# Kernel tuning notes

Measured on AMD Instinct MI355X. Metric: run time of the kernel, lower is better.

The kernel has to match this reference:

```python
import jax, jax.numpy as jnp
import numpy as np

NUM_K = 10
T = 1.0  # softmax temperature (forward default)


def setup_inputs() -> dict:
    key = jax.random.key(0)
    k1, k2, k3, k4 = jax.random.split(key, 4)
    B, H, P, D = 64, 12, 197, 64
    return {
        "att_s": jax.random.normal(k1, (B, H, P, P), dtype=jnp.float32),
        "att_t": jax.random.normal(k2, (B, H, P, P), dtype=jnp.float32),
        "v_s": jax.random.normal(k3, (B, H, P, D), dtype=jnp.float32),
        "v_t": jax.random.normal(k4, (B, H, P, D), dtype=jnp.float32),
    }


def _topk_masked_attend(att, v):
    # att: [B,H,P,P] logits, v: [B,H,P,D]
    a = jax.nn.softmax(att / T, axis=-1)
    # kth-largest value per row acts as the threshold (torch.topk semantics)
    margin = jax.lax.top_k(a, NUM_K)[0][..., -1]           # [B,H,P]
    a = a * (a >= margin[..., None])                        # keep top-k entries
    norm = a.sum(-1)                                        # [B,H,P]
    return jnp.einsum("bhpq,bhqd->bhpd", a, v) / norm[..., None]


def reference(att_s, att_t, v_s, v_t):
    out_s = _topk_masked_attend(att_s, v_s)
    out_t = _topk_masked_attend(att_t, v_t)
    # nn.MSELoss default reduction='mean'
    return jnp.mean(jnp.square(out_s - out_t))
```

## Files before the change

### kernel.cpp

```cpp
#include <hip/hip_runtime.h>
#include <cstdint>
#include <cfloat>

#define NK 10
constexpr int Pp   = 197;
constexpr int Dd   = 64;
constexpr int ROWS = 64 * 12 * 197;
constexpr int BLK  = 256;
constexpr int RPB  = 128;
constexpr int NSLAB = ROWS / RPB;
constexpr int CH   = 32;
constexpr int NCH  = Pp / CH;
constexpr int TAILC = Pp - NCH * CH;
constexpr int LDW  = CH + 4;
constexpr float INV_N = 1.0f / 9682944.0f;

constexpr int RPB_B = 16;
constexpr int NB_B  = ROWS / RPB_B;

typedef float f4 __attribute__((ext_vector_type(4), aligned(4)));

__device__ __forceinline__ uint32_t fbits(float x) { return __float_as_uint(x); }
__device__ __forceinline__ float    bfl(uint32_t u) { return __uint_as_float(u); }

__device__ __forceinline__ void pair_insert(float a[NK], float x0, float x1) {
  float u = fminf(x0, x1), v = fmaxf(x0, x1);
#pragma unroll
  for (int s = 0; s < 8; ++s) {
    float t1 = fminf(a[s + 1], v), t2 = fminf(a[s + 2], u);
    a[s] = fmaxf(fmaxf(a[s], t1), t2);
  }
  float t1 = fminf(a[9], v);
  a[8] = fmaxf(fmaxf(a[8], t1), u);
  a[9] = fmaxf(a[9], v);
}

__device__ __forceinline__ void one_insert(float a[NK], float x) {
#pragma unroll
  for (int s = 0; s < 9; ++s) a[s] = fmaxf(a[s], fminf(x, a[s + 1]));
  a[9] = fmaxf(a[9], x);
}

__device__ __forceinline__ void load_chunk(const float* __restrict__ sp, int c,
                                           int t, f4 pf[4]) {
#pragma unroll
  for (int i = 0; i < 4; ++i) {
    int f = t + BLK * i;
    int rr = f >> 3, c4 = f & 7;
    const f4* p = (const f4*)(sp + rr * Pp + c * CH + c4 * 4);
    f4 q = __builtin_nontemporal_load(p);
    uint32_t cb = (uint32_t)(c * CH + c4 * 4);
    q.x = bfl((fbits(q.x) & 0xFFFFFF00u) | cb);
    q.y = bfl((fbits(q.y) & 0xFFFFFF00u) | (cb + 1));
    q.z = bfl((fbits(q.z) & 0xFFFFFF00u) | (cb + 2));
    q.w = bfl((fbits(q.w) & 0xFFFFFF00u) | (cb + 3));
    pf[i] = q;
  }
}

__device__ __forceinline__ void load_tail(const float* __restrict__ sp, int t,
                                          float tpf[3]) {
#pragma unroll
  for (int i = 0; i < 3; ++i) {
    int e = t + BLK * i;
    if (e < RPB * TAILC) {
      int rr = e / TAILC, j = e % TAILC;
      float x = __builtin_nontemporal_load(sp + rr * Pp + NCH * CH + j);
      tpf[i] = bfl((fbits(x) & 0xFFFFFF00u) | (uint32_t)(NCH * CH + j));
    }
  }
}

__global__ __launch_bounds__(BLK, 8) void select_kernel(
    const float* __restrict__ att_s, const float* __restrict__ att_t,
    float* __restrict__ wpk ) {
  __shared__ float tile[RPB][LDW];

  const int t = threadIdx.x;
  const int bi = blockIdx.x;
  const int tensor = (bi >= NSLAB) ? 1 : 0;
  const int slab = bi - tensor * NSLAB;
  const float* A = tensor ? att_t : att_s;
  const int row0 = slab * RPB;
  const float* sp = A + (size_t)row0 * Pp;
  const int r = t >> 1, h = t & 1;

  float a[NK];
#pragma unroll
  for (int k = 0; k < NK; ++k) a[k] = -FLT_MAX;

  f4 pf[4];
  float tpf[3];
  load_chunk(sp, 0, t, pf);

  for (int c = 0; c < NCH; ++c) {
    __syncthreads();
#pragma unroll
    for (int i = 0; i < 4; ++i) {
      int f = t + BLK * i;
      *((f4*)&tile[f >> 3][(f & 7) * 4]) = pf[i];
    }
    __syncthreads();
    if (c + 1 < NCH) load_chunk(sp, c + 1, t, pf);
    else load_tail(sp, t, tpf);
#pragma unroll
    for (int j4 = 0; j4 < 4; ++j4) {
      f4 q = *((const f4*)&tile[r][16 * h + 4 * j4]);
      pair_insert(a, q.x, q.y);
      pair_insert(a, q.z, q.w);
    }
  }
  __syncthreads();
#pragma unroll
  for (int i = 0; i < 3; ++i) {
    int e = t + BLK * i;
    if (e < RPB * TAILC) tile[e / TAILC][e % TAILC] = tpf[i];
  }
  __syncthreads();
  if (h == 0) {
    pair_insert(a, tile[r][0], tile[r][1]);
    one_insert(a, tile[r][4]);
  } else {
    pair_insert(a, tile[r][2], tile[r][3]);
  }

  float b5 = __shfl_xor(a[5], 1, 64), b6 = __shfl_xor(a[6], 1, 64);
  float b7 = __shfl_xor(a[7], 1, 64), b8 = __shfl_xor(a[8], 1, 64);
  float b9 = __shfl_xor(a[9], 1, 64);
  float m[5];
  m[0] = fmaxf(a[0], b9);
  m[1] = fmaxf(a[1], b8);
  m[2] = fmaxf(a[2], b7);
  m[3] = fmaxf(a[3], b6);
  m[4] = fmaxf(a[4], b5);
  float mx = fmaxf(a[9], b9);

  float ev[5], s5 = 0.f;
#pragma unroll
  for (int i = 0; i < 5; ++i) { ev[i] = __expf(m[i] - mx); s5 += ev[i]; }
  float stot = s5 + __shfl_xor(s5, 1, 64);
  float inv = 1.0f / stot;

  float* flat = &tile[0][0];
  __syncthreads();
#pragma unroll
  for (int i = 0; i < 5; ++i) {
    float w = ev[i] * inv;
    flat[r * NK + 5 * h + i] =
        bfl((fbits(w) & 0xFFFFFF00u) | (fbits(m[i]) & 0xFFu));
  }
  __syncthreads();
  float* dst = wpk + ((size_t)tensor * ROWS + row0) * NK;
#pragma unroll
  for (int i = 0; i < 5; ++i) dst[t + BLK * i] = flat[t + BLK * i];
}

__global__ __launch_bounds__(1024) void gather_kernel(
    const float* __restrict__ v_s, const float* __restrict__ v_t,
    const float* __restrict__ wpk, float* __restrict__ partial) {
  const int t = threadIdx.x, wv = t >> 6, l = t & 63;
  int row = blockIdx.x * RPB_B + wv;
  row = __builtin_amdgcn_readfirstlane(row);
  const int bh = row / Pp;
  const float* vsb = v_s + (size_t)bh * (Pp * Dd) + l;
  const float* vtb = v_t + (size_t)bh * (Pp * Dd) + l;
  const float* w0 = wpk + (size_t)row * NK;
  const float* w1 = wpk + ((size_t)ROWS + row) * NK;

  float acc = 0.f;
#pragma unroll
  for (int k = 0; k < NK; ++k) {
    float w = w0[k];
    int idx = (int)(fbits(w) & 0xFFu);
    acc = fmaf(w, vsb[idx * Dd], acc);
  }
#pragma unroll
  for (int k = 0; k < NK; ++k) {
    float w = w1[k];
    int idx = (int)(fbits(w) & 0xFFu);
    acc = fmaf(-w, vtb[idx * Dd], acc);
  }
  float sq = acc * acc;
#pragma unroll
  for (int off = 32; off > 0; off >>= 1) sq += __shfl_xor(sq, off, 64);

  __shared__ float red[RPB_B];
  if (l == 0) red[wv] = sq;
  __syncthreads();
  if (t == 0) {
    float tot = 0.f;
#pragma unroll
    for (int i = 0; i < RPB_B; ++i) tot += red[i];
    partial[blockIdx.x] = tot;
  }
}

__global__ __launch_bounds__(1024) void reduce_kernel(
    const float* __restrict__ partial, float* __restrict__ out) {
  const int t = threadIdx.x, wv = t >> 6, l = t & 63;
  float s = 0.f;
  for (int i = t; i < NB_B; i += 1024) s += partial[i];
#pragma unroll
  for (int off = 32; off > 0; off >>= 1) s += __shfl_xor(s, off, 64);
  __shared__ float red[16];
  if (l == 0) red[wv] = s;
  __syncthreads();
  if (t == 0) {
    float tot = 0.f;
#pragma unroll
    for (int i = 0; i < 16; ++i) tot += red[i];
    out[0] = tot * INV_N;
  }
}

extern "C" void kernel_launch(void* const* d_in, const int* in_sizes, int n_in,
                              void* d_out, int out_size, void* d_ws,
                              size_t ws_size, hipStream_t stream) {
  const float* att_s = (const float*)d_in[0];
  const float* att_t = (const float*)d_in[1];
  const float* v_s = (const float*)d_in[2];
  const float* v_t = (const float*)d_in[3];
  float* out = (float*)d_out;

  float* wpk = (float*)d_ws;
  float* partial = wpk + (size_t)2 * ROWS * NK;

  select_kernel<<<2 * NSLAB, BLK, 0, stream>>>(att_s, att_t, wpk);
  gather_kernel<<<NB_B, 1024, 0, stream>>>(v_s, v_t, wpk, partial);
  reduce_kernel<<<1, 1024, 0, stream>>>(partial, out);
}
```

Measured before the change: 391.3 us.

## Load attention chunks directly into LDS and fold final reduction into gather via atomics

The select kernel now uses global_load_lds to move attention tiles straight into shared memory instead of staging them through registers, and packs the column index after the LDS read with a rotated access pattern to avoid bank conflicts. This drops the register prefetch, but loads are no longer overlapped with the compute of the previous chunk. The gather kernel becomes a fixed-size grid that processes four rows per wave with an XCD-aware block remap, and accumulates directly into the output with atomicAdd after a memset. This removes the separate reduce kernel launch and the partial-sum buffer.

```diff
diff --git a/kernel.cpp b/kernel.cpp
--- a/kernel.cpp
+++ b/kernel.cpp
@@ -12,16 +12,22 @@
 constexpr int CH   = 32;
 constexpr int NCH  = Pp / CH;
 constexpr int TAILC = Pp - NCH * CH;
-constexpr int LDW  = CH + 4;
 constexpr float INV_N = 1.0f / 9682944.0f;
 
-constexpr int RPB_B = 16;
-constexpr int NB_B  = ROWS / RPB_B;
-
-typedef float f4 __attribute__((ext_vector_type(4), aligned(4)));
+constexpr int GR_GRID = 2368;
+constexpr int GR_SLOT = GR_GRID / 8;
 
 __device__ __forceinline__ uint32_t fbits(float x) { return __float_as_uint(x); }
 __device__ __forceinline__ float    bfl(uint32_t u) { return __uint_as_float(u); }
+__device__ __forceinline__ float    packi(float x, int idx) {
+  return bfl((fbits(x) & 0xFFFFFF00u) | (uint32_t)idx);
+}
+
+__device__ __forceinline__ void gll4(const float* g, float* l) {
+  __builtin_amdgcn_global_load_lds(
+      (const __attribute__((address_space(1))) void*)g,
+      (__attribute__((address_space(3))) void*)l, 4, 0, 0);
+}
 
 __device__ __forceinline__ void pair_insert(float a[NK], float x0, float x1) {
   float u = fminf(x0, x1), v = fmaxf(x0, x1);
@@ -41,40 +47,11 @@
   a[9] = fmaxf(a[9], x);
 }
 
-__device__ __forceinline__ void load_chunk(const float* __restrict__ sp, int c,
-                                           int t, f4 pf[4]) {
-#pragma unroll
-  for (int i = 0; i < 4; ++i) {
-    int f = t + BLK * i;
-    int rr = f >> 3, c4 = f & 7;
-    const f4* p = (const f4*)(sp + rr * Pp + c * CH + c4 * 4);
-    f4 q = __builtin_nontemporal_load(p);
-    uint32_t cb = (uint32_t)(c * CH + c4 * 4);
-    q.x = bfl((fbits(q.x) & 0xFFFFFF00u) | cb);
-    q.y = bfl((fbits(q.y) & 0xFFFFFF00u) | (cb + 1));
-    q.z = bfl((fbits(q.z) & 0xFFFFFF00u) | (cb + 2));
-    q.w = bfl((fbits(q.w) & 0xFFFFFF00u) | (cb + 3));
-    pf[i] = q;
-  }
-}
-
-__device__ __forceinline__ void load_tail(const float* __restrict__ sp, int t,
-                                          float tpf[3]) {
-#pragma unroll
-  for (int i = 0; i < 3; ++i) {
-    int e = t + BLK * i;
-    if (e < RPB * TAILC) {
-      int rr = e / TAILC, j = e % TAILC;
-      float x = __builtin_nontemporal_load(sp + rr * Pp + NCH * CH + j);
-      tpf[i] = bfl((fbits(x) & 0xFFFFFF00u) | (uint32_t)(NCH * CH + j));
-    }
-  }
-}
-
 __global__ __launch_bounds__(BLK, 8) void select_kernel(
     const float* __restrict__ att_s, const float* __restrict__ att_t,
     float* __restrict__ wpk ) {
-  __shared__ float tile[RPB][LDW];
+  __shared__ float tile[RPB * CH];
+  __shared__ float ttail[RPB * TAILC];
 
   const int t = threadIdx.x;
   const int bi = blockIdx.x;
@@ -83,45 +60,54 @@
   const float* A = tensor ? att_t : att_s;
   const int row0 = slab * RPB;
   const float* sp = A + (size_t)row0 * Pp;
+
   const int r = t >> 1, h = t & 1;
+  const int r2 = (t >> 2) & 15;
+  const int w64 = t & ~63;
 
   float a[NK];
 #pragma unroll
   for (int k = 0; k < NK; ++k) a[k] = -FLT_MAX;
 
-  f4 pf[4];
-  float tpf[3];
-  load_chunk(sp, 0, t, pf);
-
   for (int c = 0; c < NCH; ++c) {
+    if (c) __syncthreads();
+#pragma unroll
+    for (int i = 0; i < 16; ++i) {
+      int f = i * BLK + t;
+      int rr = f >> 5, col = f & 31;
+      gll4(sp + rr * Pp + c * CH + col, &tile[i * BLK + w64]);
+    }
+    if (c == NCH - 1) {
+#pragma unroll
+      for (int i = 0; i < 3; ++i) {
+        int f = i * BLK + t;
+        if (f < RPB * TAILC) {
+          int rr = f / TAILC, col = f - rr * TAILC;
+          gll4(sp + rr * Pp + NCH * CH + col, &ttail[i * BLK + w64]);
+        }
+      }
+    }
     __syncthreads();
-#pragma unroll
-    for (int i = 0; i < 4; ++i) {
-      int f = t + BLK * i;
-      *((f4*)&tile[f >> 3][(f & 7) * 4]) = pf[i];
-    }
-    __syncthreads();
-    if (c + 1 < NCH) load_chunk(sp, c + 1, t, pf);
-    else load_tail(sp, t, tpf);
-#pragma unroll
-    for (int j4 = 0; j4 < 4; ++j4) {
-      f4 q = *((const f4*)&tile[r][16 * h + 4 * j4]);
-      pair_insert(a, q.x, q.y);
-      pair_insert(a, q.z, q.w);
-    }
-  }
-  __syncthreads();
-#pragma unroll
-  for (int i = 0; i < 3; ++i) {
-    int e = t + BLK * i;
-    if (e < RPB * TAILC) tile[e / TAILC][e % TAILC] = tpf[i];
-  }
-  __syncthreads();
-  if (h == 0) {
-    pair_insert(a, tile[r][0], tile[r][1]);
-    one_insert(a, tile[r][4]);
-  } else {
-    pair_insert(a, tile[r][2], tile[r][3]);
+
+    const float* trow = &tile[r * CH];
+    const int cb = c * CH + h;
+#pragma unroll
+    for (int j = 0; j < 8; ++j) {
+      int qa = (r2 + j) & 15, qb = qa ^ 8;
+      float xa = packi(trow[2 * qa + h], cb + 2 * qa);
+      float xb = packi(trow[2 * qb + h], cb + 2 * qb);
+      pair_insert(a, xa, xb);
+    }
+  }
+
+  {
+    const float* trow = &ttail[r * TAILC];
+    if (h == 0) {
+      pair_insert(a, packi(trow[0], 192), packi(trow[2], 194));
+      one_insert(a, packi(trow[4], 196));
+    } else {
+      pair_insert(a, packi(trow[1], 193), packi(trow[3], 195));
+    }
   }
 
   float b5 = __shfl_xor(a[5], 1, 64), b6 = __shfl_xor(a[6], 1, 64);
@@ -141,75 +127,61 @@
   float stot = s5 + __shfl_xor(s5, 1, 64);
   float inv = 1.0f / stot;
 
-  float* flat = &tile[0][0];
   __syncthreads();
 #pragma unroll
   for (int i = 0; i < 5; ++i) {
     float w = ev[i] * inv;
-    flat[r * NK + 5 * h + i] =
-        bfl((fbits(w) & 0xFFFFFF00u) | (fbits(m[i]) & 0xFFu));
+    tile[r * NK + 5 * h + i] = packi(w, (int)(fbits(m[i]) & 0xFFu));
   }
   __syncthreads();
   float* dst = wpk + ((size_t)tensor * ROWS + row0) * NK;
 #pragma unroll
-  for (int i = 0; i < 5; ++i) dst[t + BLK * i] = flat[t + BLK * i];
+  for (int i = 0; i < 5; ++i) dst[t + BLK * i] = tile[t + BLK * i];
 }
 
 __global__ __launch_bounds__(1024) void gather_kernel(
     const float* __restrict__ v_s, const float* __restrict__ v_t,
-    const float* __restrict__ wpk, float* __restrict__ partial) {
+    const float* __restrict__ wpk, float* __restrict__ out) {
   const int t = threadIdx.x, wv = t >> 6, l = t & 63;
-  int row = blockIdx.x * RPB_B + wv;
-  row = __builtin_amdgcn_readfirstlane(row);
-  const int bh = row / Pp;
-  const float* vsb = v_s + (size_t)bh * (Pp * Dd) + l;
-  const float* vtb = v_t + (size_t)bh * (Pp * Dd) + l;
-  const float* w0 = wpk + (size_t)row * NK;
-  const float* w1 = wpk + ((size_t)ROWS + row) * NK;
-
-  float acc = 0.f;
-#pragma unroll
-  for (int k = 0; k < NK; ++k) {
-    float w = w0[k];
-    int idx = (int)(fbits(w) & 0xFFu);
-    acc = fmaf(w, vsb[idx * Dd], acc);
-  }
-#pragma unroll
-  for (int k = 0; k < NK; ++k) {
-    float w = w1[k];
-    int idx = (int)(fbits(w) & 0xFFu);
-    acc = fmaf(-w, vtb[idx * Dd], acc);
-  }
-  float sq = acc * acc;
+  const int u = (blockIdx.x & 7) * GR_SLOT + (blockIdx.x >> 3);
+
+  float sq = 0.f;
+  for (int it = 0; it < 4; ++it) {
+    int row = u * 64 + wv * 4 + it;
+    row = __builtin_amdgcn_readfirstlane(row);
+    if (row < ROWS) {
+      const int bh = row / Pp;
+      const float* vsb = v_s + (size_t)bh * (Pp * Dd) + l;
+      const float* vtb = v_t + (size_t)bh * (Pp * Dd) + l;
+      const float* w0 = wpk + (size_t)row * NK;
+      const float* w1 = wpk + ((size_t)ROWS + row) * NK;
+      float acc = 0.f;
+#pragma unroll
+      for (int k = 0; k < NK; ++k) {
+        float w = w0[k];
+        int idx = (int)(fbits(w) & 0xFFu);
+        acc = fmaf(w, vsb[idx * Dd], acc);
+      }
+#pragma unroll
+      for (int k = 0; k < NK; ++k) {
+        float w = w1[k];
+        int idx = (int)(fbits(w) & 0xFFu);
+        acc = fmaf(-w, vtb[idx * Dd], acc);
+      }
+      sq = fmaf(acc, acc, sq);
+    }
+  }
 #pragma unroll
   for (int off = 32; off > 0; off >>= 1) sq += __shfl_xor(sq, off, 64);
 
-  __shared__ float red[RPB_B];
+  __shared__ float red[16];
   if (l == 0) red[wv] = sq;
   __syncthreads();
   if (t == 0) {
     float tot = 0.f;
 #pragma unroll
-    for (int i = 0; i < RPB_B; ++i) tot += red[i];
-    partial[blockIdx.x] = tot;
-  }
-}
-
-__global__ __launch_bounds__(1024) void reduce_kernel(
-    const float* __restrict__ partial, float* __restrict__ out) {
-  const int t = threadIdx.x, wv = t >> 6, l = t & 63;
-  float s = 0.f;
-  for (int i = t; i < NB_B; i += 1024) s += partial[i];
-#pragma unroll
-  for (int off = 32; off > 0; off >>= 1) s += __shfl_xor(s, off, 64);
-  __shared__ float red[16];
-  if (l == 0) red[wv] = s;
-  __syncthreads();
-  if (t == 0) {
-    float tot = 0.f;
-#pragma unroll
     for (int i = 0; i < 16; ++i) tot += red[i];
-    out[0] = tot * INV_N;
+    atomicAdd(out, tot * INV_N);
   }
 }
 
@@ -223,9 +195,8 @@
   float* out = (float*)d_out;
 
   float* wpk = (float*)d_ws;
-  float* partial = wpk + (size_t)2 * ROWS * NK;
-
+
+  hipMemsetAsync(out, 0, sizeof(float), stream);
   select_kernel<<<2 * NSLAB, BLK, 0, stream>>>(att_s, att_t, wpk);
-  gather_kernel<<<NB_B, 1024, 0, stream>>>(v_s, v_t, wpk, partial);
-  reduce_kernel<<<1, 1024, 0, stream>>>(partial, out);
-}
+  gather_kernel<<<GR_GRID, 1024, 0, stream>>>(v_s, v_t, wpk, out);
+}
```

Result: no change. 386.1 us (-1.3%).
